# Kernel tuning notes

Hardware: AMD Instinct MI355X
Metric: run time of the kernel (lower is better)

Reference implementation:

```python
import jax, jax.numpy as jnp
import numpy as np

D_MODEL = 1024
NUM_HEADS = 16
DEPTH = D_MODEL // NUM_HEADS


def setup_inputs() -> dict:
    key = jax.random.key(0)
    ks = jax.random.split(key, 9)
    B, S = 4, 2048
    scale = 1.0 / np.sqrt(D_MODEL)
    x = jax.random.normal(ks[0], (B, S, D_MODEL), dtype=jnp.float32)
    wq = jax.random.uniform(ks[1], (D_MODEL, D_MODEL), jnp.float32, -scale, scale)
    bq = jax.random.uniform(ks[2], (D_MODEL,), jnp.float32, -scale, scale)
    wk = jax.random.uniform(ks[3], (D_MODEL, D_MODEL), jnp.float32, -scale, scale)
    bk = jax.random.uniform(ks[4], (D_MODEL,), jnp.float32, -scale, scale)
    wv = jax.random.uniform(ks[5], (D_MODEL, D_MODEL), jnp.float32, -scale, scale)
    bv = jax.random.uniform(ks[6], (D_MODEL,), jnp.float32, -scale, scale)
    wo = jax.random.uniform(ks[7], (D_MODEL, D_MODEL), jnp.float32, -scale, scale)
    bo = jax.random.uniform(ks[8], (D_MODEL,), jnp.float32, -scale, scale)
    return {"x": x, "wq": wq, "bq": bq, "wk": wk, "bk": bk,
            "wv": wv, "bv": bv, "wo": wo, "bo": bo}


def reference(x, wq, bq, wk, bk, wv, bv, wo, bo):
    B, S, _ = x.shape
    def heads(t):  # [B,S,D] -> [B,H,S,depth]
        return t.reshape(B, S, NUM_HEADS, DEPTH).transpose(0, 2, 1, 3)
    q = heads(x @ wq + bq)
    k = heads(x @ wk + bk)
    v = heads(x @ wv + bv)
    scores = jnp.einsum('bhqd,bhkd->bhqk', q, k) / jnp.sqrt(jnp.float32(DEPTH))
    attn = jax.nn.softmax(scores, axis=-1)
    out = jnp.einsum('bhqk,bhkd->bhqd', attn, v)
    out = out.transpose(0, 2, 1, 3).reshape(B, S, D_MODEL)
    return out @ wo + bo
```

## Files before the change

kernel.cpp:

```cpp
#include <hip/hip_runtime.h>
#include <cstdint>


typedef __bf16 bf16x8 __attribute__((ext_vector_type(8)));
typedef float f32x4 __attribute__((ext_vector_type(4)));
typedef int i32x4 __attribute__((ext_vector_type(4)));

#define CEXP 0.18033688011112042f

__device__ __forceinline__ unsigned short f2bf(float f) {
  union { float f; unsigned int u; } v; v.f = f;
  unsigned int r = v.u + 0x7FFFu + ((v.u >> 16) & 1u);
  return (unsigned short)(r >> 16);
}
__device__ __forceinline__ unsigned int fbits(float f) {
  union { float f; unsigned int u; } v; v.f = f; return v.u;
}

__device__ __forceinline__ int pkbf16(float a, float b) {
#if __has_builtin(__builtin_amdgcn_cvt_pk_bf16_f32)
  auto r = __builtin_amdgcn_cvt_pk_bf16_f32(a, b);
  return __builtin_bit_cast(int, r);
#else
  return (int)__builtin_amdgcn_perm(fbits(b) + 0x8000u, fbits(a) + 0x8000u, 0x07060302u);
#endif
}

__device__ __forceinline__ void gl_lds16(const void* g, void* l) {
  __builtin_amdgcn_global_load_lds(
      (const __attribute__((address_space(1))) void*)(unsigned long long)g,
      (__attribute__((address_space(3))) void*)(unsigned int)(unsigned long long)l,
      16, 0, 0);
}

__global__ __launch_bounds__(256) void pack_all_kernel(const float* __restrict__ x,
                                                       const float* __restrict__ wq,
                                                       const float* __restrict__ wk,
                                                       const float* __restrict__ wv,
                                                       const float* __restrict__ wo,
                                                       unsigned short* __restrict__ xb,
                                                       unsigned short* __restrict__ wqkvt,
                                                       unsigned short* __restrict__ wot) {
  int bid = blockIdx.x;
  if (bid < 8192) {
    int i = (bid * 256 + threadIdx.x) * 4;
    float4 v = *(const float4*)(x + i);
    unsigned int lo = (unsigned int)f2bf(v.x) | ((unsigned int)f2bf(v.y) << 16);
    unsigned int hi = (unsigned int)f2bf(v.z) | ((unsigned int)f2bf(v.w) << 16);
    uint2 st; st.x = lo; st.y = hi;
    *(uint2*)(xb + i) = st;
    return;
  }
  __shared__ unsigned short T[64 * 66];
  bid -= 8192;
  int mat = bid >> 8;
  int tile = bid & 255;
  int tk = tile >> 4, tn = tile & 15;
  const float* W = (mat == 0) ? wq : (mat == 1) ? wk : (mat == 2) ? wv : wo;
  int t = threadIdx.x;
#pragma unroll
  for (int p = 0; p < 16; ++p) {
    int e = p * 256 + t;
    int r = e >> 6, c = e & 63;
    T[c * 66 + r] = f2bf(W[(tk * 64 + r) * 1024 + tn * 64 + c]);
  }
  __syncthreads();
  unsigned short* dst = (mat < 3) ? (wqkvt + mat * 1024 * 1024) : wot;
#pragma unroll
  for (int p = 0; p < 16; ++p) {
    int e = p * 256 + t;
    int nn = e >> 6, kk = e & 63;
    dst[(tn * 64 + nn) * 1024 + tk * 64 + kk] = T[nn * 66 + kk];
  }
}

__device__ __forceinline__ void stage_tile(const unsigned short* __restrict__ Ag,
                                           const unsigned short* __restrict__ Bg,
                                           unsigned short* As, unsigned short* Bs,
                                           int t, int wave) {
#pragma unroll
  for (int p = 0; p < 4; ++p) {
    int s = p * 256 + t;
    int row = s >> 3;
    int cc = (s & 7) ^ (row & 7);
    gl_lds16(Ag + row * 1024 + cc * 8, (void*)(As + (p * 256 + wave * 64) * 8));
    gl_lds16(Bg + row * 1024 + cc * 8, (void*)(Bs + (p * 256 + wave * 64) * 8));
  }
}

template <int MODE>
__global__ __launch_bounds__(256) void gemm_bt_kernel(
    const unsigned short* __restrict__ A, const unsigned short* __restrict__ Bt,
    const float* __restrict__ b0, const float* __restrict__ b1, const float* __restrict__ b2,
    unsigned short* __restrict__ Qg, unsigned short* __restrict__ Kg,
    unsigned short* __restrict__ Vtg, float* __restrict__ Of) {
  __shared__ __align__(16) unsigned short S[32768];
  const int t = threadIdx.x;
  const int lane = t & 63, wave = t >> 6;
  const int l15 = lane & 15, quad = lane >> 4;
  const int wm = wave & 1, wn = wave >> 1;
  const int m0 = blockIdx.x * 128, n0 = blockIdx.y * 128;
  const unsigned short* Ab = A + (size_t)m0 * 1024;
  const unsigned short* Bb = Bt + (size_t)n0 * 1024;

  f32x4 acc[4][4];
#pragma unroll
  for (int i = 0; i < 4; ++i)
#pragma unroll
    for (int j = 0; j < 4; ++j) acc[i][j] = (f32x4){0.f, 0.f, 0.f, 0.f};

  const int Xo0 = ((quad ^ (l15 & 7)) * 8);
  const int Xo1 = (((4 + quad) ^ (l15 & 7)) * 8);

  stage_tile(Ab, Bb, S, S + 8192, t, wave);

  for (int k0 = 0; k0 < 1024; k0 += 64) {
    const int buf = (k0 >> 6) & 1;
    unsigned short* Sc = S + buf * 16384;
    __syncthreads();
    if (k0 < 1024 - 64) {
      unsigned short* Sn = S + (buf ^ 1) * 16384;
      stage_tile(Ab + k0 + 64, Bb + k0 + 64, Sn, Sn + 8192, t, wave);
    }
#pragma unroll
    for (int kc = 0; kc < 2; ++kc) {
      const int Xo = kc ? Xo1 : Xo0;
      bf16x8 af[4], bfr[4];
#pragma unroll
      for (int mi = 0; mi < 4; ++mi)
        af[mi] = *(const bf16x8*)&Sc[(wm * 64 + mi * 16 + l15) * 64 + Xo];
#pragma unroll
      for (int ni = 0; ni < 4; ++ni)
        bfr[ni] = *(const bf16x8*)&Sc[8192 + (wn * 64 + ni * 16 + l15) * 64 + Xo];
#pragma unroll
      for (int mi = 0; mi < 4; ++mi)
#pragma unroll
        for (int ni = 0; ni < 4; ++ni)
          acc[mi][ni] = __builtin_amdgcn_mfma_f32_16x16x32_bf16(af[mi], bfr[ni], acc[mi][ni], 0, 0, 0);
    }
  }

  if (MODE == 0) {
    const int seg = blockIdx.y >> 3;
    const float* bias = (seg == 0) ? b0 : (seg == 1) ? b1 : b2;
    unsigned short* qk = (seg == 0) ? Qg : Kg;
#pragma unroll
    for (int mi = 0; mi < 4; ++mi)
#pragma unroll
      for (int ni = 0; ni < 4; ++ni) {
        int n = n0 + wn * 64 + ni * 16 + l15;
        int nn = n & 1023;
        float bb = bias[nn];
        int h = nn >> 6, d = nn & 63;
#pragma unroll
        for (int r = 0; r < 4; ++r) {
          int m = m0 + wm * 64 + mi * 16 + quad * 4 + r;
          int b = m >> 11, s = m & 2047;
          float val = acc[mi][ni][r] + bb;
          if (seg == 2) {
            int sp = (s & ~63) | (s & 32) | ((s & 12) << 1) | ((s & 16) >> 2) | (s & 3);
            Vtg[((b * 16 + h) * 64 + d) * 2048 + sp] = f2bf(val);
          } else {
            if (seg == 0) val *= CEXP;
            qk[((b * 16 + h) * 2048 + s) * 64 + d] = f2bf(val);
          }
        }
      }
  } else {
#pragma unroll
    for (int mi = 0; mi < 4; ++mi)
#pragma unroll
      for (int ni = 0; ni < 4; ++ni) {
        int n = n0 + wn * 64 + ni * 16 + l15;
        float bb = b0[n];
#pragma unroll
        for (int r = 0; r < 4; ++r) {
          int m = m0 + wm * 64 + mi * 16 + quad * 4 + r;
          Of[m * 1024 + n] = acc[mi][ni][r] + bb;
        }
      }
  }
}

__global__ __launch_bounds__(256) void attn_kernel(const unsigned short* __restrict__ Qg,
                                                   const unsigned short* __restrict__ Kg,
                                                   const unsigned short* __restrict__ Vtg,
                                                   unsigned short* __restrict__ Og) {
  __shared__ __align__(16) unsigned short smem[16384];
  const int t = threadIdx.x;
  const int lane = t & 63, wave = t >> 6;
  const int l15 = lane & 15, quad = lane >> 4;
  const int bid = blockIdx.x;
  const int bh = (bid & 7) * 8 + (bid >> 7);
  const int qt = (bid >> 3) & 15;

  const unsigned short* Qh = Qg + (bh * 2048 + qt * 128) * 64;
  const unsigned short* Kh = Kg + bh * 2048 * 64;
  const unsigned short* Vth = Vtg + bh * 64 * 2048;

#pragma unroll
  for (int p = 0; p < 4; ++p) {
    int s = p * 256 + t;
    int row = s >> 3, cc = (s & 7) ^ (row & 7);
    gl_lds16(Qh + row * 64 + cc * 8, (void*)(smem + (p * 256 + wave * 64) * 8));
  }
  __syncthreads();

  const int Xo0 = ((quad ^ (l15 & 7)) * 8);
  const int Xo1 = (((4 + quad) ^ (l15 & 7)) * 8);

  bf16x8 qf[2][2];
#pragma unroll
  for (int qi = 0; qi < 2; ++qi) {
    qf[qi][0] = *(const bf16x8*)&smem[(wave * 32 + qi * 16 + l15) * 64 + Xo0];
    qf[qi][1] = *(const bf16x8*)&smem[(wave * 32 + qi * 16 + l15) * 64 + Xo1];
  }

#pragma unroll
  for (int p = 0; p < 2; ++p) {
    int s = p * 256 + t;
    int row = s >> 3, cc = (s & 7) ^ (row & 7);
    gl_lds16(Kh + row * 64 + cc * 8, (void*)(smem + 8192 + (p * 256 + wave * 64) * 8));
    gl_lds16(Vth + row * 2048 + cc * 8, (void*)(smem + 12288 + (p * 256 + wave * 64) * 8));
  }

  const f32x4 FZ = (f32x4){0.f, 0.f, 0.f, 0.f};
  const int one2 = 0x3F803F80;
  const i32x4 onesi = (i32x4){one2, one2, one2, one2};
  const bf16x8 ones = __builtin_bit_cast(bf16x8, onesi);

  f32x4 oacc[4][2];
#pragma unroll
  for (int di = 0; di < 4; ++di)
#pragma unroll
    for (int qi = 0; qi < 2; ++qi) oacc[di][qi] = FZ;
  f32x4 lacc[2];
  lacc[0] = FZ; lacc[1] = FZ;

  for (int kt = 0; kt < 32; ++kt) {
    __syncthreads();
    if (kt + 1 < 32) {
      const unsigned short* Kn = Kh + (kt + 1) * 64 * 64;
      const unsigned short* Vn = Vth + (kt + 1) * 64;
      unsigned short* Kd = smem + (((kt + 1) & 1) ? 0 : 8192);
      unsigned short* Vd = smem + (((kt + 1) & 1) ? 4096 : 12288);
#pragma unroll
      for (int p = 0; p < 2; ++p) {
        int s = p * 256 + t;
        int row = s >> 3, cc = (s & 7) ^ (row & 7);
        gl_lds16(Kn + row * 64 + cc * 8, (void*)(Kd + (p * 256 + wave * 64) * 8));
        gl_lds16(Vn + row * 2048 + cc * 8, (void*)(Vd + (p * 256 + wave * 64) * 8));
      }
    }
    const unsigned short* Ks = smem + ((kt & 1) ? 0 : 8192);
    const unsigned short* Vs = smem + ((kt & 1) ? 4096 : 12288);

    f32x4 sacc[4][2];
    {
      bf16x8 kf[4];
#pragma unroll
      for (int ki = 0; ki < 4; ++ki)
        kf[ki] = *(const bf16x8*)&Ks[(ki * 16 + l15) * 64 + Xo0];
#pragma unroll
      for (int ki = 0; ki < 4; ++ki)
#pragma unroll
        for (int qi = 0; qi < 2; ++qi)
          sacc[ki][qi] = __builtin_amdgcn_mfma_f32_16x16x32_bf16(kf[ki], qf[qi][0], FZ, 0, 0, 0);
#pragma unroll
      for (int ki = 0; ki < 4; ++ki)
        kf[ki] = *(const bf16x8*)&Ks[(ki * 16 + l15) * 64 + Xo1];
#pragma unroll
      for (int ki = 0; ki < 4; ++ki)
#pragma unroll
        for (int qi = 0; qi < 2; ++qi)
          sacc[ki][qi] = __builtin_amdgcn_mfma_f32_16x16x32_bf16(kf[ki], qf[qi][1], sacc[ki][qi], 0, 0, 0);
    }

    i32x4 pk[2][2];
#pragma unroll
    for (int qi = 0; qi < 2; ++qi)
#pragma unroll
      for (int kc = 0; kc < 2; ++kc)
#pragma unroll
        for (int u = 0; u < 2; ++u) {
          int ki = kc * 2 + u;
          float p0 = __builtin_amdgcn_exp2f(sacc[ki][qi][0]);
          float p1 = __builtin_amdgcn_exp2f(sacc[ki][qi][1]);
          float p2 = __builtin_amdgcn_exp2f(sacc[ki][qi][2]);
          float p3 = __builtin_amdgcn_exp2f(sacc[ki][qi][3]);
          pk[qi][kc][u * 2 + 0] = pkbf16(p0, p1);
          pk[qi][kc][u * 2 + 1] = pkbf16(p2, p3);
        }

#pragma unroll
    for (int kc = 0; kc < 2; ++kc) {
      const int Xo = kc ? Xo1 : Xo0;
      bf16x8 vf[4];
#pragma unroll
      for (int di = 0; di < 4; ++di)
        vf[di] = *(const bf16x8*)&Vs[(di * 16 + l15) * 64 + Xo];
#pragma unroll
      for (int di = 0; di < 4; ++di)
#pragma unroll
        for (int qi = 0; qi < 2; ++qi)
          oacc[di][qi] = __builtin_amdgcn_mfma_f32_16x16x32_bf16(
              vf[di], __builtin_bit_cast(bf16x8, pk[qi][kc]), oacc[di][qi], 0, 0, 0);
#pragma unroll
      for (int qi = 0; qi < 2; ++qi)
        lacc[qi] = __builtin_amdgcn_mfma_f32_16x16x32_bf16(
            ones, __builtin_bit_cast(bf16x8, pk[qi][kc]), lacc[qi], 0, 0, 0);
    }
  }

  const int b = bh >> 4, h = bh & 15;
#pragma unroll
  for (int qi = 0; qi < 2; ++qi) {
    float inv = 1.f / lacc[qi][0];
    int q = qt * 128 + wave * 32 + qi * 16 + l15;
#pragma unroll
    for (int di = 0; di < 4; ++di) {
      unsigned int lo = (unsigned int)f2bf(oacc[di][qi][0] * inv) |
                        ((unsigned int)f2bf(oacc[di][qi][1] * inv) << 16);
      unsigned int hi = (unsigned int)f2bf(oacc[di][qi][2] * inv) |
                        ((unsigned int)f2bf(oacc[di][qi][3] * inv) << 16);
      uint2 st; st.x = lo; st.y = hi;
      *(uint2*)(Og + ((size_t)(b * 2048 + q) * 1024) + h * 64 + di * 16 + quad * 4) = st;
    }
  }
}

extern "C" void kernel_launch(void* const* d_in, const int* in_sizes, int n_in,
                              void* d_out, int out_size, void* d_ws, size_t ws_size,
                              hipStream_t stream) {
  const float* x  = (const float*)d_in[0];
  const float* wq = (const float*)d_in[1];
  const float* bq = (const float*)d_in[2];
  const float* wk = (const float*)d_in[3];
  const float* bk = (const float*)d_in[4];
  const float* wv = (const float*)d_in[5];
  const float* bv = (const float*)d_in[6];
  const float* wo = (const float*)d_in[7];
  const float* bo = (const float*)d_in[8];
  char* ws = (char*)d_ws;
  unsigned short* Xb    = (unsigned short*)(ws);
  unsigned short* Wqkvt = (unsigned short*)(ws + (16ull << 20));
  unsigned short* Wot   = (unsigned short*)(ws + (22ull << 20));
  unsigned short* Qg    = (unsigned short*)(ws + (24ull << 20));
  unsigned short* Kg    = (unsigned short*)(ws + (40ull << 20));
  unsigned short* Vtg   = (unsigned short*)(ws + (56ull << 20));
  unsigned short* Og    = (unsigned short*)(ws + (72ull << 20));

  pack_all_kernel<<<9216, 256, 0, stream>>>(x, wq, wk, wv, wo, Xb, Wqkvt, Wot);
  gemm_bt_kernel<0><<<dim3(64, 24), 256, 0, stream>>>(Xb, Wqkvt, bq, bk, bv,
                                                      Qg, Kg, Vtg, nullptr);
  attn_kernel<<<1024, 256, 0, stream>>>(Qg, Kg, Vtg, Og);
  gemm_bt_kernel<1><<<dim3(64, 8), 256, 0, stream>>>(Og, Wot, bo, nullptr, nullptr,
                                                     nullptr, nullptr, nullptr,
                                                     (float*)d_out);
}
```

Measured before the change: 291.2 us.

## Software-pipeline PV matmul behind next QK tile and vectorize GEMM epilogue stores

The attention loop now computes the PV product for the previous key tile while the current tile's QK scores are computed, using triple-buffered V tiles in shared memory so the exp2 and MFMA work can overlap. Q staging moves to a separate region, which enlarges shared memory. The GEMM swaps its MFMA operand order (transposed accumulators) for the Q/K and output projections, so each lane holds four consecutive columns and can issue vectorized bias loads and packed or float4 stores instead of scalar ones. V keeps the original order so its transposed layout also gets packed stores. The cost is more LDS per block, which may lower occupancy, and higher register pressure from carrying P values across iterations.

```diff
diff --git a/kernel.cpp b/kernel.cpp
--- a/kernel.cpp
+++ b/kernel.cpp
@@ -88,6 +88,42 @@
   }
 }
 
+template <int TRANS>
+__device__ __forceinline__ void kloop(const unsigned short* __restrict__ Ab,
+                                      const unsigned short* __restrict__ Bb,
+                                      unsigned short* S, f32x4 acc[4][4],
+                                      int t, int wave, int l15, int quad,
+                                      int wm, int wn, int Xo0, int Xo1) {
+  stage_tile(Ab, Bb, S, S + 8192, t, wave);
+  for (int k0 = 0; k0 < 1024; k0 += 64) {
+    const int buf = (k0 >> 6) & 1;
+    unsigned short* Sc = S + buf * 16384;
+    __syncthreads();
+    if (k0 < 1024 - 64) {
+      unsigned short* Sn = S + (buf ^ 1) * 16384;
+      stage_tile(Ab + k0 + 64, Bb + k0 + 64, Sn, Sn + 8192, t, wave);
+    }
+#pragma unroll
+    for (int kc = 0; kc < 2; ++kc) {
+      const int Xo = kc ? Xo1 : Xo0;
+      bf16x8 af[4], bfr[4];
+#pragma unroll
+      for (int mi = 0; mi < 4; ++mi)
+        af[mi] = *(const bf16x8*)&Sc[(wm * 64 + mi * 16 + l15) * 64 + Xo];
+#pragma unroll
+      for (int ni = 0; ni < 4; ++ni)
+        bfr[ni] = *(const bf16x8*)&Sc[8192 + (wn * 64 + ni * 16 + l15) * 64 + Xo];
+#pragma unroll
+      for (int mi = 0; mi < 4; ++mi)
+#pragma unroll
+        for (int ni = 0; ni < 4; ++ni)
+          acc[mi][ni] = TRANS
+              ? __builtin_amdgcn_mfma_f32_16x16x32_bf16(bfr[ni], af[mi], acc[mi][ni], 0, 0, 0)
+              : __builtin_amdgcn_mfma_f32_16x16x32_bf16(af[mi], bfr[ni], acc[mi][ni], 0, 0, 0);
+    }
+  }
+}
+
 template <int MODE>
 __global__ __launch_bounds__(256) void gemm_bt_kernel(
     const unsigned short* __restrict__ A, const unsigned short* __restrict__ Bt,
@@ -102,6 +138,7 @@
   const int m0 = blockIdx.x * 128, n0 = blockIdx.y * 128;
   const unsigned short* Ab = A + (size_t)m0 * 1024;
   const unsigned short* Bb = Bt + (size_t)n0 * 1024;
+  const int seg = (MODE == 0) ? (blockIdx.y >> 3) : 0;
 
   f32x4 acc[4][4];
 #pragma unroll
@@ -112,73 +149,69 @@
   const int Xo0 = ((quad ^ (l15 & 7)) * 8);
   const int Xo1 = (((4 + quad) ^ (l15 & 7)) * 8);
 
-  stage_tile(Ab, Bb, S, S + 8192, t, wave);
-
-  for (int k0 = 0; k0 < 1024; k0 += 64) {
-    const int buf = (k0 >> 6) & 1;
-    unsigned short* Sc = S + buf * 16384;
-    __syncthreads();
-    if (k0 < 1024 - 64) {
-      unsigned short* Sn = S + (buf ^ 1) * 16384;
-      stage_tile(Ab + k0 + 64, Bb + k0 + 64, Sn, Sn + 8192, t, wave);
-    }
-#pragma unroll
-    for (int kc = 0; kc < 2; ++kc) {
-      const int Xo = kc ? Xo1 : Xo0;
-      bf16x8 af[4], bfr[4];
-#pragma unroll
-      for (int mi = 0; mi < 4; ++mi)
-        af[mi] = *(const bf16x8*)&Sc[(wm * 64 + mi * 16 + l15) * 64 + Xo];
-#pragma unroll
-      for (int ni = 0; ni < 4; ++ni)
-        bfr[ni] = *(const bf16x8*)&Sc[8192 + (wn * 64 + ni * 16 + l15) * 64 + Xo];
-#pragma unroll
-      for (int mi = 0; mi < 4; ++mi)
-#pragma unroll
-        for (int ni = 0; ni < 4; ++ni)
-          acc[mi][ni] = __builtin_amdgcn_mfma_f32_16x16x32_bf16(af[mi], bfr[ni], acc[mi][ni], 0, 0, 0);
-    }
-  }
-
-  if (MODE == 0) {
-    const int seg = blockIdx.y >> 3;
-    const float* bias = (seg == 0) ? b0 : (seg == 1) ? b1 : b2;
-    unsigned short* qk = (seg == 0) ? Qg : Kg;
-#pragma unroll
-    for (int mi = 0; mi < 4; ++mi)
-#pragma unroll
-      for (int ni = 0; ni < 4; ++ni) {
-        int n = n0 + wn * 64 + ni * 16 + l15;
-        int nn = n & 1023;
-        float bb = bias[nn];
-        int h = nn >> 6, d = nn & 63;
-#pragma unroll
-        for (int r = 0; r < 4; ++r) {
-          int m = m0 + wm * 64 + mi * 16 + quad * 4 + r;
-          int b = m >> 11, s = m & 2047;
-          float val = acc[mi][ni][r] + bb;
-          if (seg == 2) {
-            int sp = (s & ~63) | (s & 32) | ((s & 12) << 1) | ((s & 16) >> 2) | (s & 3);
-            Vtg[((b * 16 + h) * 64 + d) * 2048 + sp] = f2bf(val);
-          } else {
-            if (seg == 0) val *= CEXP;
-            qk[((b * 16 + h) * 2048 + s) * 64 + d] = f2bf(val);
-          }
+  if (MODE == 1 || seg < 2) {
+    kloop<1>(Ab, Bb, S, acc, t, wave, l15, quad, wm, wn, Xo0, Xo1);
+    if (MODE == 0) {
+      const float* bias = (seg == 0) ? b0 : b1;
+      unsigned short* qk = (seg == 0) ? Qg : Kg;
+      const int m = m0 + wm * 64 + l15;
+#pragma unroll
+      for (int mi = 0; mi < 4; ++mi) {
+        int mm = m + mi * 16;
+        int b = mm >> 11, s = mm & 2047;
+        size_t rowoff;
+#pragma unroll
+        for (int ni = 0; ni < 4; ++ni) {
+          int nb = n0 + wn * 64 + ni * 16 + quad * 4;
+          int nn = nb & 1023;
+          float4 bb = *(const float4*)(bias + nn);
+          int h = nn >> 6, d = nn & 63;
+          float v0 = acc[mi][ni][0] + bb.x, v1 = acc[mi][ni][1] + bb.y;
+          float v2 = acc[mi][ni][2] + bb.z, v3 = acc[mi][ni][3] + bb.w;
+          if (seg == 0) { v0 *= CEXP; v1 *= CEXP; v2 *= CEXP; v3 *= CEXP; }
+          uint2 st;
+          st.x = (unsigned int)pkbf16(v0, v1);
+          st.y = (unsigned int)pkbf16(v2, v3);
+          *(uint2*)(qk + ((size_t)((b * 16 + h) * 2048 + s)) * 64 + d) = st;
         }
       }
-  } else {
-#pragma unroll
-    for (int mi = 0; mi < 4; ++mi)
-#pragma unroll
-      for (int ni = 0; ni < 4; ++ni) {
-        int n = n0 + wn * 64 + ni * 16 + l15;
-        float bb = b0[n];
-#pragma unroll
-        for (int r = 0; r < 4; ++r) {
-          int m = m0 + wm * 64 + mi * 16 + quad * 4 + r;
-          Of[m * 1024 + n] = acc[mi][ni][r] + bb;
+    } else {
+      const int m = m0 + wm * 64 + l15;
+#pragma unroll
+      for (int mi = 0; mi < 4; ++mi) {
+        int mm = m + mi * 16;
+#pragma unroll
+        for (int ni = 0; ni < 4; ++ni) {
+          int n = n0 + wn * 64 + ni * 16 + quad * 4;
+          float4 bb = *(const float4*)(b0 + n);
+          float4 st;
+          st.x = acc[mi][ni][0] + bb.x; st.y = acc[mi][ni][1] + bb.y;
+          st.z = acc[mi][ni][2] + bb.z; st.w = acc[mi][ni][3] + bb.w;
+          *(float4*)(Of + (size_t)mm * 1024 + n) = st;
         }
       }
+    }
+  } else {
+    kloop<0>(Ab, Bb, S, acc, t, wave, l15, quad, wm, wn, Xo0, Xo1);
+#pragma unroll
+    for (int ni = 0; ni < 4; ++ni) {
+      int n = n0 + wn * 64 + ni * 16 + l15;
+      int nn = n & 1023;
+      int h = nn >> 6, d = nn & 63;
+      float bb = b2[nn];
+#pragma unroll
+      for (int mi = 0; mi < 4; ++mi) {
+        int mb = m0 + wm * 64 + mi * 16 + quad * 4;
+        int b = mb >> 11, s0 = mb & 2047;
+        int sp0 = (s0 & ~63) | (s0 & 32) | ((s0 & 12) << 1) | ((s0 & 16) >> 2);
+        float v0 = acc[mi][ni][0] + bb, v1 = acc[mi][ni][1] + bb;
+        float v2 = acc[mi][ni][2] + bb, v3 = acc[mi][ni][3] + bb;
+        uint2 st;
+        st.x = (unsigned int)pkbf16(v0, v1);
+        st.y = (unsigned int)pkbf16(v2, v3);
+        *(uint2*)(Vtg + ((size_t)((b * 16 + h) * 64 + d)) * 2048 + sp0) = st;
+      }
+    }
   }
 }
 
@@ -186,7 +219,7 @@
                                                    const unsigned short* __restrict__ Kg,
                                                    const unsigned short* __restrict__ Vtg,
                                                    unsigned short* __restrict__ Og) {
-  __shared__ __align__(16) unsigned short smem[16384];
+  __shared__ __align__(16) unsigned short smem[20480];
   const int t = threadIdx.x;
   const int lane = t & 63, wave = t >> 6;
   const int l15 = lane & 15, quad = lane >> 4;
@@ -202,27 +235,27 @@
   for (int p = 0; p < 4; ++p) {
     int s = p * 256 + t;
     int row = s >> 3, cc = (s & 7) ^ (row & 7);
-    gl_lds16(Qh + row * 64 + cc * 8, (void*)(smem + (p * 256 + wave * 64) * 8));
-  }
-  __syncthreads();
-
-  const int Xo0 = ((quad ^ (l15 & 7)) * 8);
-  const int Xo1 = (((4 + quad) ^ (l15 & 7)) * 8);
-
-  bf16x8 qf[2][2];
-#pragma unroll
-  for (int qi = 0; qi < 2; ++qi) {
-    qf[qi][0] = *(const bf16x8*)&smem[(wave * 32 + qi * 16 + l15) * 64 + Xo0];
-    qf[qi][1] = *(const bf16x8*)&smem[(wave * 32 + qi * 16 + l15) * 64 + Xo1];
-  }
-
+    gl_lds16(Qh + row * 64 + cc * 8, (void*)(smem + 12288 + (p * 256 + wave * 64) * 8));
+  }
 #pragma unroll
   for (int p = 0; p < 2; ++p) {
     int s = p * 256 + t;
     int row = s >> 3, cc = (s & 7) ^ (row & 7);
-    gl_lds16(Kh + row * 64 + cc * 8, (void*)(smem + 8192 + (p * 256 + wave * 64) * 8));
-    gl_lds16(Vth + row * 2048 + cc * 8, (void*)(smem + 12288 + (p * 256 + wave * 64) * 8));
-  }
+    gl_lds16(Kh + row * 64 + cc * 8, (void*)(smem + (p * 256 + wave * 64) * 8));
+    gl_lds16(Vth + row * 2048 + cc * 8, (void*)(smem + 8192 + (p * 256 + wave * 64) * 8));
+  }
+  __syncthreads();
+
+  const int Xo0 = ((quad ^ (l15 & 7)) * 8);
+  const int Xo1 = (((4 + quad) ^ (l15 & 7)) * 8);
+
+  bf16x8 qf[2][2];
+#pragma unroll
+  for (int qi = 0; qi < 2; ++qi) {
+    qf[qi][0] = *(const bf16x8*)&smem[12288 + (wave * 32 + qi * 16 + l15) * 64 + Xo0];
+    qf[qi][1] = *(const bf16x8*)&smem[12288 + (wave * 32 + qi * 16 + l15) * 64 + Xo1];
+  }
+  __syncthreads();
 
   const f32x4 FZ = (f32x4){0.f, 0.f, 0.f, 0.f};
   const int one2 = 0x3F803F80;
@@ -237,23 +270,25 @@
   f32x4 lacc[2];
   lacc[0] = FZ; lacc[1] = FZ;
 
+  i32x4 pkP[2][2];
+  int kCur = 0, kNxt = 4096;
+  int vPrv = 16384, vCur = 8192, vNxt = 12288;
+
   for (int kt = 0; kt < 32; ++kt) {
-    __syncthreads();
-    if (kt + 1 < 32) {
+    if (kt) __syncthreads();
+    if (kt < 31) {
       const unsigned short* Kn = Kh + (kt + 1) * 64 * 64;
       const unsigned short* Vn = Vth + (kt + 1) * 64;
-      unsigned short* Kd = smem + (((kt + 1) & 1) ? 0 : 8192);
-      unsigned short* Vd = smem + (((kt + 1) & 1) ? 4096 : 12288);
 #pragma unroll
       for (int p = 0; p < 2; ++p) {
         int s = p * 256 + t;
         int row = s >> 3, cc = (s & 7) ^ (row & 7);
-        gl_lds16(Kn + row * 64 + cc * 8, (void*)(Kd + (p * 256 + wave * 64) * 8));
-        gl_lds16(Vn + row * 2048 + cc * 8, (void*)(Vd + (p * 256 + wave * 64) * 8));
+        gl_lds16(Kn + row * 64 + cc * 8, (void*)(smem + kNxt + (p * 256 + wave * 64) * 8));
+        gl_lds16(Vn + row * 2048 + cc * 8, (void*)(smem + vNxt + (p * 256 + wave * 64) * 8));
       }
     }
-    const unsigned short* Ks = smem + ((kt & 1) ? 0 : 8192);
-    const unsigned short* Vs = smem + ((kt & 1) ? 4096 : 12288);
+    const unsigned short* Ks = smem + kCur;
+    const unsigned short* Vp = smem + vPrv;
 
     f32x4 sacc[4][2];
     {
@@ -276,7 +311,27 @@
           sacc[ki][qi] = __builtin_amdgcn_mfma_f32_16x16x32_bf16(kf[ki], qf[qi][1], sacc[ki][qi], 0, 0, 0);
     }
 
-    i32x4 pk[2][2];
+    if (kt > 0) {
+#pragma unroll
+      for (int kc = 0; kc < 2; ++kc) {
+        const int Xo = kc ? Xo1 : Xo0;
+        bf16x8 vf[4];
+#pragma unroll
+        for (int di = 0; di < 4; ++di)
+          vf[di] = *(const bf16x8*)&Vp[(di * 16 + l15) * 64 + Xo];
+#pragma unroll
+        for (int di = 0; di < 4; ++di)
+#pragma unroll
+          for (int qi = 0; qi < 2; ++qi)
+            oacc[di][qi] = __builtin_amdgcn_mfma_f32_16x16x32_bf16(
+                vf[di], __builtin_bit_cast(bf16x8, pkP[qi][kc]), oacc[di][qi], 0, 0, 0);
+#pragma unroll
+        for (int qi = 0; qi < 2; ++qi)
+          lacc[qi] = __builtin_amdgcn_mfma_f32_16x16x32_bf16(
+              ones, __builtin_bit_cast(bf16x8, pkP[qi][kc]), lacc[qi], 0, 0, 0);
+      }
+    }
+
 #pragma unroll
     for (int qi = 0; qi < 2; ++qi)
 #pragma unroll
@@ -288,27 +343,33 @@
           float p1 = __builtin_amdgcn_exp2f(sacc[ki][qi][1]);
           float p2 = __builtin_amdgcn_exp2f(sacc[ki][qi][2]);
           float p3 = __builtin_amdgcn_exp2f(sacc[ki][qi][3]);
-          pk[qi][kc][u * 2 + 0] = pkbf16(p0, p1);
-          pk[qi][kc][u * 2 + 1] = pkbf16(p2, p3);
+          pkP[qi][kc][u * 2 + 0] = pkbf16(p0, p1);
+          pkP[qi][kc][u * 2 + 1] = pkbf16(p2, p3);
         }
 
+    int tmp = kCur; kCur = kNxt; kNxt = tmp;
+    tmp = vPrv; vPrv = vCur; vCur = vNxt; vNxt = tmp;
+  }
+
+  {
+    const unsigned short* Vp = smem + vPrv;
 #pragma unroll
     for (int kc = 0; kc < 2; ++kc) {
       const int Xo = kc ? Xo1 : Xo0;
       bf16x8 vf[4];
 #pragma unroll
       for (int di = 0; di < 4; ++di)
-        vf[di] = *(const bf16x8*)&Vs[(di * 16 + l15) * 64 + Xo];
+        vf[di] = *(const bf16x8*)&Vp[(di * 16 + l15) * 64 + Xo];
 #pragma unroll
       for (int di = 0; di < 4; ++di)
 #pragma unroll
         for (int qi = 0; qi < 2; ++qi)
           oacc[di][qi] = __builtin_amdgcn_mfma_f32_16x16x32_bf16(
-              vf[di], __builtin_bit_cast(bf16x8, pk[qi][kc]), oacc[di][qi], 0, 0, 0);
+              vf[di], __builtin_bit_cast(bf16x8, pkP[qi][kc]), oacc[di][qi], 0, 0, 0);
 #pragma unroll
       for (int qi = 0; qi < 2; ++qi)
         lacc[qi] = __builtin_amdgcn_mfma_f32_16x16x32_bf16(
-            ones, __builtin_bit_cast(bf16x8, pk[qi][kc]), lacc[qi], 0, 0, 0);
+            ones, __builtin_bit_cast(bf16x8, pkP[qi][kc]), lacc[qi], 0, 0, 0);
     }
   }
 
```

After: 267.9 us. -8.0%, faster.
